# Performance work log

Hardware: AMD Instinct MI355X
Metric: run time of the kernel (lower is better)

The kernel has to match this reference:

```python
import jax, jax.numpy as jnp
import numpy as np

R = 32          # voxel_resolution
GN_GROUPS = 8   # GroupNorm groups used throughout the module


def group_norm(x, scale, bias, groups, eps=1e-5):
    B, C = x.shape[0], x.shape[1]
    spatial = x.shape[2:]
    xg = x.reshape(B, groups, C // groups, -1)
    mu = xg.mean(axis=(2, 3), keepdims=True)
    var = xg.var(axis=(2, 3), keepdims=True)
    xn = ((xg - mu) / jnp.sqrt(var + eps)).reshape((B, C) + spatial)
    sh = (1, C) + (1,) * len(spatial)
    return xn * scale.reshape(sh) + bias.reshape(sh)


def conv3d_same(x, w, b):
    pad = w.shape[-1] // 2
    y = jax.lax.conv_general_dilated(
        x, w, (1, 1, 1), [(pad, pad)] * 3,
        dimension_numbers=('NCDHW', 'OIDHW', 'NCDHW'))
    return y + b.reshape(1, -1, 1, 1, 1)


def _voxelize(coords, features, r):
    # PVCNN Voxelization: center coords, normalize to [0,1], scale to grid,
    # scatter-MEAN point features into a dense [B,C,r,r,r] grid.
    B, C, N = features.shape
    centered = coords - coords.mean(axis=2, keepdims=True)            # [B,3,N]
    norm = jnp.linalg.norm(centered, axis=1, keepdims=True)           # [B,1,N]
    denom = norm.max(axis=2, keepdims=True) * 2.0                     # eps = 0
    nc = centered / denom + 0.5
    nc = jnp.clip(nc * r, 0.0, r - 1.0)                               # float voxel coords
    vi = jnp.round(nc).astype(jnp.int32)                              # [B,3,N]
    flat = (vi[:, 0] * r + vi[:, 1]) * r + vi[:, 2]                   # [B,N]
    seg = (flat + (jnp.arange(B, dtype=jnp.int32) * (r ** 3))[:, None]).reshape(-1)
    feats = features.transpose(0, 2, 1).reshape(B * N, C)
    sums = jax.ops.segment_sum(feats, seg, num_segments=B * r ** 3)
    cnts = jax.ops.segment_sum(jnp.ones((B * N,), feats.dtype), seg,
                               num_segments=B * r ** 3)
    mean = sums / jnp.maximum(cnts, 1.0)[:, None]
    grid = mean.reshape(B, r, r, r, C).transpose(0, 4, 1, 2, 3)       # [B,C,r,r,r]
    return nc, grid


def _trilinear_devoxelize(nc, grid, r):
    # nc [B,3,N] float in [0,r-1]; grid [B,C,r,r,r] -> gather 8 corners + weights
    B, C = grid.shape[0], grid.shape[1]
    lo = jnp.floor(nc)
    frac = nc - lo                                                    # [B,3,N]
    lo_i = lo.astype(jnp.int32)
    hi_i = jnp.minimum(lo_i + 1, r - 1)
    gf = grid.reshape(B, C, r * r * r)
    out = jnp.zeros((B, C, nc.shape[2]), grid.dtype)
    for dx in (0, 1):
        for dy in (0, 1):
            for dz in (0, 1):
                ix = hi_i[:, 0] if dx else lo_i[:, 0]
                iy = hi_i[:, 1] if dy else lo_i[:, 1]
                iz = hi_i[:, 2] if dz else lo_i[:, 2]
                w = ((frac[:, 0] if dx else 1.0 - frac[:, 0]) *
                     (frac[:, 1] if dy else 1.0 - frac[:, 1]) *
                     (frac[:, 2] if dz else 1.0 - frac[:, 2]))        # [B,N]
                idx = (ix * r + iy) * r + iz                          # [B,N]
                g = jnp.take_along_axis(gf, idx[:, None, :], axis=2)  # [B,C,N]
                out = out + g * w[:, None, :]
    return out


def setup_inputs() -> dict:
    key = jax.random.key(0)
    ks = jax.random.split(key, 6)
    B, N, Cin, Cout, K = 4, 65536, 64, 128, 3
    return {
        'coords':   jax.random.normal(ks[0], (B, 3, N), jnp.float32),
        'features': jax.random.normal(ks[1], (B, Cin, N), jnp.float32),
        'conv1_w':  jax.random.normal(ks[2], (Cout, Cin, K, K, K), jnp.float32) * 0.02,
        'conv1_b':  jnp.zeros((Cout,), jnp.float32),
        'gn1_scale': jnp.ones((Cout,), jnp.float32),
        'gn1_bias':  jnp.zeros((Cout,), jnp.float32),
        'conv2_w':  jax.random.normal(ks[3], (Cout, Cout, K, K, K), jnp.float32) * 0.02,
        'conv2_b':  jnp.zeros((Cout,), jnp.float32),
        'gn2_scale': jnp.ones((Cout,), jnp.float32),
        'gn2_bias':  jnp.zeros((Cout,), jnp.float32),
        'point_w':  jax.random.normal(ks[4], (Cout, Cin), jnp.float32) * 0.05,
        'point_b':  jnp.zeros((Cout,), jnp.float32),
        'point_gn_scale': jnp.ones((Cout,), jnp.float32),
        'point_gn_bias':  jnp.zeros((Cout,), jnp.float32),
    }


def reference(coords, features, conv1_w, conv1_b, gn1_scale, gn1_bias,
              conv2_w, conv2_b, gn2_scale, gn2_bias,
              point_w, point_b, point_gn_scale, point_gn_bias):
    nc, grid = _voxelize(coords, features, R)
    # voxel branch: Conv3d -> GN -> SiLU -> (dropout, eval: identity) -> Conv3d -> GN -> SiLU
    h = conv3d_same(grid, conv1_w, conv1_b)
    h = jax.nn.silu(group_norm(h, gn1_scale, gn1_bias, GN_GROUPS))
    h = conv3d_same(h, conv2_w, conv2_b)
    h = jax.nn.silu(group_norm(h, gn2_scale, gn2_bias, GN_GROUPS))
    # point branch: SharedMLP = 1x1 Conv1d -> GN -> SiLU
    p = jnp.einsum('oc,bcn->bon', point_w, features) + point_b[None, :, None]
    p = jax.nn.silu(group_norm(p, point_gn_scale, point_gn_bias, GN_GROUPS))
    vpts = _trilinear_devoxelize(nc, h, R)                            # [B,Cout,N]
    return p + vpts
```

## Files before the change

### kernel.cpp

```cpp
#include <hip/hip_runtime.h>

typedef __attribute__((ext_vector_type(8))) short bf16x8;
typedef __attribute__((ext_vector_type(4))) float f32x4;
typedef __attribute__((ext_vector_type(4))) int i32x4;
typedef __attribute__((ext_vector_type(2))) int i32x2;

#define B_ 4
#define N_ 65536
#define RRR_ 32768
#define PADV_ 39304
#define PPLANE_ 1156

static const size_t OFF_NC     = 0;
static const size_t OFF_VIDX   = 786432;
static const size_t OFF_WT1    = 1048576;
static const size_t OFF_WT2    = 1159168;
static const size_t OFF_C2OUT  = 1380352;
static const size_t OFF_CNT    = 9768960;
static const size_t OFF_GSUM   = 9900032;
static const size_t OFF_GPAD   = 18288640;
static const size_t OFF_ACT1   = 23319552;
static const size_t OFF_GSTATS = 33381376;
static const size_t OFF_BSTATS = 33381568;
static const size_t MEMSET_FLOATS = 33381584 - 9768960;

__device__ __forceinline__ ushort f2bf(float x) {
    union { float f; unsigned u; } c; c.f = x;
    unsigned r = c.u + 0x7fffu + ((c.u >> 16) & 1u);
    return (ushort)(r >> 16);
}
__device__ __forceinline__ float bf2f(ushort h) {
    union { unsigned u; float f; } c; c.u = ((unsigned)h) << 16;
    return c.f;
}

__global__ __launch_bounds__(256) void k_coord_sum(const float* __restrict__ coords,
                                                   float* __restrict__ bstats) {
    int b = blockIdx.y;
    int tid = threadIdx.x;
    const float* cb = coords + (size_t)b * 3 * N_;
    float s0 = 0.f, s1 = 0.f, s2 = 0.f;
    for (int n = blockIdx.x * 256 + tid; n < N_; n += 64 * 256) {
        s0 += cb[n]; s1 += cb[N_ + n]; s2 += cb[2 * N_ + n];
    }
    #pragma unroll
    for (int off = 1; off < 64; off <<= 1) {
        s0 += __shfl_xor(s0, off);
        s1 += __shfl_xor(s1, off);
        s2 += __shfl_xor(s2, off);
    }
    if ((tid & 63) == 0) {
        atomicAdd(&bstats[b * 4 + 0], s0);
        atomicAdd(&bstats[b * 4 + 1], s1);
        atomicAdd(&bstats[b * 4 + 2], s2);
    }
}

__global__ __launch_bounds__(256) void k_coord_max(const float* __restrict__ coords,
                                                   float* __restrict__ bstats) {
    int b = blockIdx.y;
    int tid = threadIdx.x;
    const float invN = 1.0f / (float)N_;
    float m0 = bstats[b * 4 + 0] * invN;
    float m1 = bstats[b * 4 + 1] * invN;
    float m2 = bstats[b * 4 + 2] * invN;
    const float* cb = coords + (size_t)b * 3 * N_;
    float mx = 0.f;
    for (int n = blockIdx.x * 256 + tid; n < N_; n += 64 * 256) {
        float x = cb[n] - m0, y = cb[N_ + n] - m1, z = cb[2 * N_ + n] - m2;
        mx = fmaxf(mx, x * x + y * y + z * z);
    }
    #pragma unroll
    for (int off = 1; off < 64; off <<= 1)
        mx = fmaxf(mx, __shfl_xor(mx, off));
    if ((tid & 63) == 0)
        atomicMax((int*)&bstats[b * 4 + 3], __float_as_int(mx));
}

__global__ __launch_bounds__(256) void k_point_prep(const float* __restrict__ coords,
                                                    const float* __restrict__ bstats,
                                                    float* __restrict__ nc,
                                                    int* __restrict__ vidx,
                                                    float* __restrict__ cnt) {
    int gid = blockIdx.x * 256 + threadIdx.x;
    int b = gid >> 16;
    int n = gid & (N_ - 1);
    const float invN = 1.0f / (float)N_;
    float m[3] = {bstats[b * 4 + 0] * invN, bstats[b * 4 + 1] * invN, bstats[b * 4 + 2] * invN};
    float den = 2.0f * sqrtf(__int_as_float(((const int*)bstats)[b * 4 + 3]));
    const float* cb = coords + (size_t)b * 3 * N_;
    int vi[3];
    #pragma unroll
    for (int d = 0; d < 3; ++d) {
        float cv = cb[(size_t)d * N_ + n];
        float t = (cv - m[d]) / den + 0.5f;
        t *= 32.0f;
        t = fminf(fmaxf(t, 0.0f), 31.0f);
        nc[((size_t)b * 3 + d) * N_ + n] = t;
        vi[d] = (int)rintf(t);
    }
    int flat = (vi[0] * 32 + vi[1]) * 32 + vi[2];
    vidx[(b << 16) + n] = flat;
    atomicAdd(&cnt[(b << 15) + flat], 1.0f);
}

__global__ __launch_bounds__(256) void k_scatter_cl(const float* __restrict__ feats,
                                                    const int* __restrict__ vidx,
                                                    float* __restrict__ gsum) {
    __shared__ float lf[64 * 129];
    __shared__ int sidx[128];
    int tid = threadIdx.x;
    int b = blockIdx.y;
    int n0 = blockIdx.x * 128;
    for (int i = tid; i < 64 * 128; i += 256) {
        int ci = i >> 7, pt = i & 127;
        lf[ci * 129 + pt] = feats[((size_t)(b * 64 + ci)) * N_ + n0 + pt];
    }
    if (tid < 128) sidx[tid] = vidx[(b << 16) + n0 + tid];
    __syncthreads();
    for (int i = tid; i < 64 * 128; i += 256) {
        int ci = i & 63, pt = i >> 6;
        atomicAdd(&gsum[((size_t)(b << 15) + sidx[pt]) * 64 + ci], lf[ci * 129 + pt]);
    }
}

__global__ __launch_bounds__(256) void k_gridmean_cl(const float* __restrict__ gsum,
                                                     const float* __restrict__ cnt,
                                                     ushort* __restrict__ gpad) {
    int idx = blockIdx.x * 256 + threadIdx.x;
    int q = idx & 15;
    int vox = (idx >> 4) & 32767;
    int b = idx >> 19;
    float c = cnt[(b << 15) + vox];
    float inv = 1.0f / fmaxf(c, 1.0f);
    float4 v = *(const float4*)(gsum + (((size_t)(b << 15) + vox) << 6) + q * 4);
    int zz = vox >> 10, yy = (vox >> 5) & 31, xx = vox & 31;
    size_t o = ((size_t)b * PADV_ + (size_t)(zz + 1) * PPLANE_ + (yy + 1) * 34 + (xx + 1)) * 64 + q * 4;
    i32x2 pk;
    ushort* u = (ushort*)&pk;
    u[0] = f2bf(v.x * inv); u[1] = f2bf(v.y * inv);
    u[2] = f2bf(v.z * inv); u[3] = f2bf(v.w * inv);
    *(i32x2*)(gpad + o) = pk;
}

template <int CI>
__global__ __launch_bounds__(256) void k_wtrans(const float* __restrict__ w,
                                                ushort* __restrict__ wt) {
    int idx = blockIdx.x * 256 + threadIdx.x;
    if (idx >= 27 * 128 * CI) return;
    int tap = idx / (128 * CI);
    int rem = idx - tap * 128 * CI;
    int co = rem / CI;
    int ci = rem - co * CI;
    wt[idx] = f2bf(w[((size_t)co * CI + ci) * 27 + tap]);
}

template <int CI, bool PAD_OUT>
__global__ __launch_bounds__(512, 2) void k_conv(const ushort* __restrict__ inp,
                                                 const ushort* __restrict__ wt,
                                                 const float* __restrict__ bias,
                                                 ushort* __restrict__ outp,
                                                 float* __restrict__ gstats,
                                                 int layer) {
    constexpr int NK = 27 * CI / 64;
    __shared__ i32x4 lds_mem[6144];
    char* lds = (char*)lds_mem;

    const int yg = blockIdx.x, z0 = blockIdx.y, b = blockIdx.z;
    const int y0 = yg * 8;
    const int tid = threadIdx.x;
    const int w = tid >> 6, l = tid & 63;
    const int lk = l >> 4, lr = l & 15;
    const int wr = w >> 1, wc = w & 1;

    const ushort* actb = inp + (size_t)b * PADV_ * CI;

    int aglb[4], awld[4];
    #pragma unroll
    for (int i = 0; i < 4; ++i) {
        int idx = tid + i * 512;
        int row = idx >> 3, j = idx & 7;
        int py = row >> 5, px = row & 31;
        aglb[i] = (z0 * PPLANE_ + (y0 + py) * 34 + px) * CI + j * 8;
        awld[i] = row * 128 + ((j ^ (row & 7)) << 4);
    }
    int bglb[2], bwld[2];
    #pragma unroll
    for (int i = 0; i < 2; ++i) {
        int idx = tid + i * 512;
        int co = idx >> 3, j = idx & 7;
        bglb[i] = co * CI + j * 8;
        bwld[i] = co * 128 + ((j ^ (co & 7)) << 4);
    }
    int ard[4][2], brd[4][2];
    #pragma unroll
    for (int i = 0; i < 4; ++i) {
        int pos = wr * 64 + i * 16 + lr;
        #pragma unroll
        for (int kk = 0; kk < 2; ++kk)
            ard[i][kk] = pos * 128 + (((kk * 4 + lk) ^ (pos & 7)) << 4);
    }
    #pragma unroll
    for (int n = 0; n < 4; ++n) {
        int co = wc * 64 + n * 16 + lr;
        #pragma unroll
        for (int kk = 0; kk < 2; ++kk)
            brd[n][kk] = co * 128 + (((kk * 4 + lk) ^ (co & 7)) << 4);
    }

    f32x4 acc[4][4];
    #pragma unroll
    for (int i = 0; i < 4; ++i)
        #pragma unroll
        for (int n = 0; n < 4; ++n)
            acc[i][n] = (f32x4){0.f, 0.f, 0.f, 0.f};

    i32x4 ar[4], br[2];
    #pragma unroll
    for (int i = 0; i < 4; ++i) ar[i] = *(const i32x4*)(actb + aglb[i]);
    #pragma unroll
    for (int i = 0; i < 2; ++i) br[i] = *(const i32x4*)(wt + bglb[i]);
    #pragma unroll
    for (int i = 0; i < 4; ++i) *(i32x4*)(lds + awld[i]) = ar[i];
    #pragma unroll
    for (int i = 0; i < 2; ++i) *(i32x4*)(lds + 65536 + bwld[i]) = br[i];
    __syncthreads();

    #pragma unroll 2
    for (int ks = 0; ks < NK; ++ks) {
        const int cur = ks & 1;
        const bool more = (ks + 1 < NK);
        if (more) {
            int ksn = ks + 1;
            int tap = (CI == 64) ? ksn : (ksn >> 1);
            int choff = (CI == 64) ? 0 : ((ksn & 1) << 6);
            int fz = tap / 9, r9 = tap - fz * 9;
            int fy = r9 / 3, fx = r9 - fy * 3;
            int adelta = (fz * PPLANE_ + fy * 34 + fx) * CI + choff;
            const ushort* wp = wt + tap * (128 * CI) + choff;
            #pragma unroll
            for (int i = 0; i < 4; ++i) ar[i] = *(const i32x4*)(actb + aglb[i] + adelta);
            #pragma unroll
            for (int i = 0; i < 2; ++i) br[i] = *(const i32x4*)(wp + bglb[i]);
        }
        const char* Ac = lds + cur * 32768;
        const char* Bc = lds + 65536 + cur * 16384;
        #pragma unroll
        for (int kk = 0; kk < 2; ++kk) {
            bf16x8 af[4], bfr[4];
            #pragma unroll
            for (int i = 0; i < 4; ++i) af[i] = *(const bf16x8*)(Ac + ard[i][kk]);
            #pragma unroll
            for (int n = 0; n < 4; ++n) bfr[n] = *(const bf16x8*)(Bc + brd[n][kk]);
            #pragma unroll
            for (int i = 0; i < 4; ++i)
                #pragma unroll
                for (int n = 0; n < 4; ++n)
                    acc[i][n] = __builtin_amdgcn_mfma_f32_16x16x32_bf16(af[i], bfr[n], acc[i][n], 0, 0, 0);
        }
        if (more) {
            char* An = lds + (cur ^ 1) * 32768;
            char* Bn = lds + 65536 + (cur ^ 1) * 16384;
            #pragma unroll
            for (int i = 0; i < 4; ++i) *(i32x4*)(An + awld[i]) = ar[i];
            #pragma unroll
            for (int i = 0; i < 2; ++i) *(i32x4*)(Bn + bwld[i]) = br[i];
            __syncthreads();
        }
    }

    __syncthreads();
    ushort* outs = (ushort*)lds;
    float bb[4];
    #pragma unroll
    for (int n = 0; n < 4; ++n) bb[n] = bias[wc * 64 + n * 16 + lr];
    float sg[4] = {0.f, 0.f, 0.f, 0.f}, sq[4] = {0.f, 0.f, 0.f, 0.f};
    #pragma unroll
    for (int i = 0; i < 4; ++i) {
        int posb = wr * 64 + i * 16 + lk * 4;
        #pragma unroll
        for (int n = 0; n < 4; ++n) {
            int co = wc * 64 + n * 16 + lr;
            #pragma unroll
            for (int r = 0; r < 4; ++r) {
                float v = acc[i][n][r] + bb[n];
                sg[n] += v; sq[n] += v * v;
                outs[(posb + r) * 128 + co] = f2bf(v);
            }
        }
    }
    #pragma unroll
    for (int off = 1; off < 64; off <<= 1) {
        #pragma unroll
        for (int n = 0; n < 4; ++n) {
            sg[n] += __shfl_xor(sg[n], off);
            sq[n] += __shfl_xor(sq[n], off);
        }
    }
    if (l == 0) {
        int gbase = layer * 32 + b * 8 + wc * 4;
        #pragma unroll
        for (int n = 0; n < 4; ++n) {
            atomicAdd(&gstats[(gbase + n) * 2 + 0], sg[n]);
            atomicAdd(&gstats[(gbase + n) * 2 + 1], sq[n]);
        }
    }
    __syncthreads();
    for (int idx = tid; idx < 4096; idx += 512) {
        int pos = idx >> 4, c8 = idx & 15;
        int yy = y0 + (pos >> 5), xx = pos & 31;
        size_t g;
        if (PAD_OUT)
            g = ((size_t)b * PADV_ + (size_t)(z0 + 1) * PPLANE_ + (yy + 1) * 34 + (xx + 1)) * 128 + c8 * 8;
        else
            g = ((size_t)b * RRR_ + z0 * 1024 + yy * 32 + xx) * 128 + c8 * 8;
        *(i32x4*)(outp + g) = *((i32x4*)lds + idx);
    }
}

template <bool PAD>
__global__ __launch_bounds__(256) void k_gn_apply(ushort* __restrict__ x,
                                                  const float* __restrict__ gstats,
                                                  const float* __restrict__ sc,
                                                  const float* __restrict__ bi,
                                                  int layer, float invc) {
    int idx = blockIdx.x * 256 + threadIdx.x;
    int c8 = idx & 15;
    int vox = (idx >> 4) & 32767;
    int b = idx >> 19;
    size_t base;
    if (PAD) {
        int zz = vox >> 10, yy = (vox >> 5) & 31, xx = vox & 31;
        base = ((size_t)b * PADV_ + (size_t)(zz + 1) * PPLANE_ + (yy + 1) * 34 + (xx + 1)) * 128 + c8 * 8;
    } else {
        base = ((size_t)b * RRR_ + vox) * 128 + c8 * 8;
    }
    int g = c8 >> 1;
    float sum = gstats[(layer * 32 + b * 8 + g) * 2 + 0];
    float ssq = gstats[(layer * 32 + b * 8 + g) * 2 + 1];
    float mean = sum * invc;
    float var = ssq * invc - mean * mean;
    float rstd = rsqrtf(var + 1e-5f);
    i32x4 raw = *(i32x4*)(x + base);
    ushort* u = (ushort*)&raw;
    #pragma unroll
    for (int j = 0; j < 8; ++j) {
        int co = c8 * 8 + j;
        float v = bf2f(u[j]);
        v = (v - mean) * rstd * sc[co] + bi[co];
        v = v / (1.f + __expf(-v));
        u[j] = f2bf(v);
    }
    *(i32x4*)(x + base) = raw;
}

__global__ __launch_bounds__(256) void k_point_mlp(const float* __restrict__ feats,
                                                   const float* __restrict__ w,
                                                   const float* __restrict__ pb,
                                                   float* __restrict__ out,
                                                   float* __restrict__ gstats) {
    __shared__ float wl[64 * 132];
    __shared__ float sred[4][16];
    int tid = threadIdx.x;
    for (int i = tid; i < 128 * 64; i += 256) {
        int o = i >> 6, c = i & 63;
        wl[c * 132 + o] = w[i];
    }
    __syncthreads();
    int gid = blockIdx.x * 256 + tid;
    int b = gid >> 16, n = gid & (N_ - 1);
    const float* fb = feats + (size_t)b * 64 * N_ + n;
    float acc[128];
    #pragma unroll
    for (int o = 0; o < 128; ++o) acc[o] = 0.f;
    for (int c = 0; c < 64; ++c) {
        float f = fb[(size_t)c * N_];
        const float4* wr4 = (const float4*)&wl[c * 132];
        #pragma unroll
        for (int o4 = 0; o4 < 32; ++o4) {
            float4 wv = wr4[o4];
            acc[4 * o4 + 0] = fmaf(f, wv.x, acc[4 * o4 + 0]);
            acc[4 * o4 + 1] = fmaf(f, wv.y, acc[4 * o4 + 1]);
            acc[4 * o4 + 2] = fmaf(f, wv.z, acc[4 * o4 + 2]);
            acc[4 * o4 + 3] = fmaf(f, wv.w, acc[4 * o4 + 3]);
        }
    }
    float* ob = out + (size_t)b * 128 * N_ + n;
    float sg[8] = {0.f}, sq[8] = {0.f};
    #pragma unroll
    for (int o = 0; o < 128; ++o) {
        float v = acc[o] + pb[o];
        ob[(size_t)o * N_] = v;
        sg[o >> 4] += v;
        sq[o >> 4] += v * v;
    }
    #pragma unroll
    for (int off = 1; off < 64; off <<= 1) {
        #pragma unroll
        for (int g = 0; g < 8; ++g) {
            sg[g] += __shfl_xor(sg[g], off);
            sq[g] += __shfl_xor(sq[g], off);
        }
    }
    int wv = tid >> 6, l = tid & 63;
    if (l == 0) {
        #pragma unroll
        for (int g = 0; g < 8; ++g) { sred[wv][g] = sg[g]; sred[wv][8 + g] = sq[g]; }
    }
    __syncthreads();
    if (tid < 16) {
        float v = sred[0][tid] + sred[1][tid] + sred[2][tid] + sred[3][tid];
        int g = tid & 7, part = tid >> 3;
        atomicAdd(&gstats[(64 + b * 8 + g) * 2 + part], v);
    }
}

__global__ __launch_bounds__(256) void k_devox_final(const float* __restrict__ nc,
                                                     const ushort* __restrict__ ht,
                                                     const float* __restrict__ gstats,
                                                     const float* __restrict__ scale,
                                                     const float* __restrict__ bias,
                                                     float* __restrict__ out) {
    __shared__ float vp[64][129];
    __shared__ int sidx[64][8];
    __shared__ float swt[64][8];
    int tid = threadIdx.x;
    int blk = blockIdx.x;
    int b = blk >> 10;
    int n0 = (blk & 1023) * 64;
    if (tid < 64) {
        int n = n0 + tid;
        float f0 = nc[(size_t)b * 3 * N_ + n];
        float f1 = nc[((size_t)b * 3 + 1) * N_ + n];
        float f2 = nc[((size_t)b * 3 + 2) * N_ + n];
        float l0 = floorf(f0), l1 = floorf(f1), l2 = floorf(f2);
        float r0 = f0 - l0, r1 = f1 - l1, r2 = f2 - l2;
        int i0 = (int)l0, i1 = (int)l1, i2 = (int)l2;
        int h0 = min(i0 + 1, 31), h1 = min(i1 + 1, 31), h2 = min(i2 + 1, 31);
        #pragma unroll
        for (int k = 0; k < 8; ++k) {
            int dx = (k >> 2) & 1, dy = (k >> 1) & 1, dz = k & 1;
            int ix = dx ? h0 : i0, iy = dy ? h1 : i1, iz = dz ? h2 : i2;
            float w = (dx ? r0 : 1.f - r0) * (dy ? r1 : 1.f - r1) * (dz ? r2 : 1.f - r2);
            sidx[tid][k] = (ix * 32 + iy) * 32 + iz;
            swt[tid][k] = w;
        }
    }
    __syncthreads();
    const ushort* hb = ht + (size_t)b * RRR_ * 128;
    for (int t = tid; t < 64 * 16; t += 256) {
        int c8 = t & 15, pt = t >> 4;
        float a[8] = {0.f, 0.f, 0.f, 0.f, 0.f, 0.f, 0.f, 0.f};
        #pragma unroll
        for (int k = 0; k < 8; ++k) {
            i32x4 raw = *(const i32x4*)(hb + (size_t)sidx[pt][k] * 128 + c8 * 8);
            ushort* u = (ushort*)&raw;
            float wk = swt[pt][k];
            #pragma unroll
            for (int j = 0; j < 8; ++j)
                a[j] = fmaf(wk, bf2f(u[j]), a[j]);
        }
        #pragma unroll
        for (int j = 0; j < 8; ++j)
            vp[pt][c8 * 8 + j] = a[j];
    }
    __syncthreads();
    const float invc = 1.0f / (16.0f * (float)N_);
    for (int t = tid; t < 64 * 128; t += 256) {
        int nl = t & 63;
        int c = t >> 6;
        int g = c >> 4;
        float sum = gstats[(64 + b * 8 + g) * 2 + 0];
        float ssq = gstats[(64 + b * 8 + g) * 2 + 1];
        float mean = sum * invc;
        float var = ssq * invc - mean * mean;
        float rstd = rsqrtf(var + 1e-5f);
        size_t o = ((size_t)(b * 128 + c)) * N_ + n0 + nl;
        float v = (out[o] - mean) * rstd * scale[c] + bias[c];
        v = v / (1.f + __expf(-v));
        out[o] = v + vp[nl][c];
    }
}

extern "C" void kernel_launch(void* const* d_in, const int* in_sizes, int n_in,
                              void* d_out, int out_size, void* d_ws, size_t ws_size,
                              hipStream_t stream) {
    const float* coords   = (const float*)d_in[0];
    const float* features = (const float*)d_in[1];
    const float* conv1_w  = (const float*)d_in[2];
    const float* conv1_b  = (const float*)d_in[3];
    const float* gn1_s    = (const float*)d_in[4];
    const float* gn1_b    = (const float*)d_in[5];
    const float* conv2_w  = (const float*)d_in[6];
    const float* conv2_b  = (const float*)d_in[7];
    const float* gn2_s    = (const float*)d_in[8];
    const float* gn2_b    = (const float*)d_in[9];
    const float* point_w  = (const float*)d_in[10];
    const float* point_b  = (const float*)d_in[11];
    const float* pgn_s    = (const float*)d_in[12];
    const float* pgn_b    = (const float*)d_in[13];
    float* out = (float*)d_out;
    float* ws = (float*)d_ws;

    float*  nc     = ws + OFF_NC;
    int*    vidx   = (int*)(ws + OFF_VIDX);
    ushort* wt1    = (ushort*)(ws + OFF_WT1);
    ushort* wt2    = (ushort*)(ws + OFF_WT2);
    ushort* c2out  = (ushort*)(ws + OFF_C2OUT);
    float*  cnt    = ws + OFF_CNT;
    float*  gsum   = ws + OFF_GSUM;
    ushort* gpad   = (ushort*)(ws + OFF_GPAD);
    ushort* act1   = (ushort*)(ws + OFF_ACT1);
    float*  gstats = ws + OFF_GSTATS;
    float*  bstats = ws + OFF_BSTATS;

    const float invc = 1.0f / (float)(RRR_ * 16);

    hipMemsetAsync(cnt, 0, MEMSET_FLOATS * sizeof(float), stream);

    k_coord_sum<<<dim3(64, B_), 256, 0, stream>>>(coords, bstats);
    k_coord_max<<<dim3(64, B_), 256, 0, stream>>>(coords, bstats);
    k_point_prep<<<B_ * N_ / 256, 256, 0, stream>>>(coords, bstats, nc, vidx, cnt);
    k_scatter_cl<<<dim3(N_ / 128, B_), 256, 0, stream>>>(features, vidx, gsum);
    k_gridmean_cl<<<B_ * RRR_ * 16 / 256, 256, 0, stream>>>(gsum, cnt, gpad);

    k_wtrans<64><<<(27 * 128 * 64 + 255) / 256, 256, 0, stream>>>(conv1_w, wt1);
    k_wtrans<128><<<(27 * 128 * 128 + 255) / 256, 256, 0, stream>>>(conv2_w, wt2);

    k_conv<64, true><<<dim3(4, 32, B_), 512, 0, stream>>>(gpad, wt1, conv1_b, act1, gstats, 0);
    k_gn_apply<true><<<B_ * RRR_ * 16 / 256, 256, 0, stream>>>(act1, gstats, gn1_s, gn1_b, 0, invc);

    k_conv<128, false><<<dim3(4, 32, B_), 512, 0, stream>>>(act1, wt2, conv2_b, c2out, gstats, 1);
    k_gn_apply<false><<<B_ * RRR_ * 16 / 256, 256, 0, stream>>>(c2out, gstats, gn2_s, gn2_b, 1, invc);

    k_point_mlp<<<B_ * N_ / 256, 256, 0, stream>>>(features, point_w, point_b, out, gstats);
    k_devox_final<<<B_ * N_ / 64, 256, 0, stream>>>(nc, c2out, gstats, pgn_s, pgn_b, out);
}
```

Before: 1.011 ms.

## Stage conv tiles via direct global-to-LDS loads with pre-swizzled weights

The implicit-GEMM 3D conv now loads activation and weight tiles directly into LDS with global_load_lds instead of staging them through registers. Weights are pre-arranged in the XOR-swizzled order so each thread copies a contiguous 16-byte chunk. The block tile drops from 256 to 128 positions with 256 threads, halving LDS use and doubling the grid. This removes register staging and LDS store instructions, but relies on vmcnt waits plus a barrier every k-step and gives less reuse of each weight tile per block.

```diff
diff --git a/kernel.cpp b/kernel.cpp
--- a/kernel.cpp
+++ b/kernel.cpp
@@ -32,6 +32,13 @@
 __device__ __forceinline__ float bf2f(ushort h) {
     union { unsigned u; float f; } c; c.u = ((unsigned)h) << 16;
     return c.f;
+}
+
+__device__ __forceinline__ void gl16(const void* g, void* l) {
+    __builtin_amdgcn_global_load_lds(
+        (const __attribute__((address_space(1))) unsigned int*)(g),
+        (__attribute__((address_space(3))) unsigned int*)(l),
+        16, 0, 0);
 }
 
 __global__ __launch_bounds__(256) void k_coord_sum(const float* __restrict__ coords,
@@ -148,50 +155,48 @@
                                                 ushort* __restrict__ wt) {
     int idx = blockIdx.x * 256 + threadIdx.x;
     if (idx >= 27 * 128 * CI) return;
-    int tap = idx / (128 * CI);
-    int rem = idx - tap * 128 * CI;
-    int co = rem / CI;
-    int ci = rem - co * CI;
+    int e = idx & 7;
+    int jm = (idx >> 3) & 7;
+    int co = (idx >> 6) & 127;
+    int ks = idx >> 13;
+    int q = jm ^ (co & 7);
+    int tap = (CI == 64) ? ks : (ks >> 1);
+    int ci = ((CI == 64) ? 0 : ((ks & 1) * 64)) + q * 8 + e;
     wt[idx] = f2bf(w[((size_t)co * CI + ci) * 27 + tap]);
 }
 
 template <int CI, bool PAD_OUT>
-__global__ __launch_bounds__(512, 2) void k_conv(const ushort* __restrict__ inp,
+__global__ __launch_bounds__(256, 2) void k_conv(const ushort* __restrict__ inp,
                                                  const ushort* __restrict__ wt,
                                                  const float* __restrict__ bias,
                                                  ushort* __restrict__ outp,
                                                  float* __restrict__ gstats,
                                                  int layer) {
     constexpr int NK = 27 * CI / 64;
-    __shared__ i32x4 lds_mem[6144];
-    char* lds = (char*)lds_mem;
+    __shared__ char lds[65536];
 
     const int yg = blockIdx.x, z0 = blockIdx.y, b = blockIdx.z;
-    const int y0 = yg * 8;
+    const int y0 = yg * 4;
     const int tid = threadIdx.x;
     const int w = tid >> 6, l = tid & 63;
     const int lk = l >> 4, lr = l & 15;
     const int wr = w >> 1, wc = w & 1;
 
-    const ushort* actb = inp + (size_t)b * PADV_ * CI;
-
-    int aglb[4], awld[4];
+    const char* actb = (const char*)(inp + (size_t)b * PADV_ * CI);
+    const char* wtb = (const char*)wt;
+
+    const char* agp[4];
     #pragma unroll
     for (int i = 0; i < 4; ++i) {
-        int idx = tid + i * 512;
-        int row = idx >> 3, j = idx & 7;
+        int s = tid + i * 256;
+        int row = s >> 3, j = s & 7;
+        int jj = j ^ (row & 7);
         int py = row >> 5, px = row & 31;
-        aglb[i] = (z0 * PPLANE_ + (y0 + py) * 34 + px) * CI + j * 8;
-        awld[i] = row * 128 + ((j ^ (row & 7)) << 4);
-    }
-    int bglb[2], bwld[2];
-    #pragma unroll
-    for (int i = 0; i < 2; ++i) {
-        int idx = tid + i * 512;
-        int co = idx >> 3, j = idx & 7;
-        bglb[i] = co * CI + j * 8;
-        bwld[i] = co * 128 + ((j ^ (co & 7)) << 4);
-    }
+        agp[i] = actb + ((size_t)(z0 * PPLANE_ + (y0 + py) * 34 + px) * CI) * 2 + jj * 16;
+    }
+    char* ldsAw = lds + w * 1024;
+    char* ldsBw = lds + 32768 + w * 1024;
+
     int ard[4][2], brd[4][2];
     #pragma unroll
     for (int i = 0; i < 4; ++i) {
@@ -215,36 +220,31 @@
         for (int n = 0; n < 4; ++n)
             acc[i][n] = (f32x4){0.f, 0.f, 0.f, 0.f};
 
-    i32x4 ar[4], br[2];
-    #pragma unroll
-    for (int i = 0; i < 4; ++i) ar[i] = *(const i32x4*)(actb + aglb[i]);
-    #pragma unroll
-    for (int i = 0; i < 2; ++i) br[i] = *(const i32x4*)(wt + bglb[i]);
-    #pragma unroll
-    for (int i = 0; i < 4; ++i) *(i32x4*)(lds + awld[i]) = ar[i];
-    #pragma unroll
-    for (int i = 0; i < 2; ++i) *(i32x4*)(lds + 65536 + bwld[i]) = br[i];
+    auto stage = [&](int ks, int cur) {
+        int tap = (CI == 64) ? ks : (ks >> 1);
+        int choff2 = (CI == 64) ? 0 : ((ks & 1) << 7);
+        int fz = tap / 9, r9 = tap - fz * 9;
+        int fy = r9 / 3, fx = r9 - fy * 3;
+        int ad = (fz * PPLANE_ + fy * 34 + fx) * CI * 2 + choff2;
+        #pragma unroll
+        for (int i = 0; i < 4; ++i)
+            gl16(agp[i] + ad, ldsAw + cur * 16384 + i * 4096);
+        const char* wsrc = wtb + (size_t)ks * 16384 + tid * 16;
+        #pragma unroll
+        for (int i = 0; i < 4; ++i)
+            gl16(wsrc + i * 4096, ldsBw + cur * 16384 + i * 4096);
+    };
+
+    stage(0, 0);
+    asm volatile("s_waitcnt vmcnt(0)" ::: "memory");
     __syncthreads();
 
     #pragma unroll 2
     for (int ks = 0; ks < NK; ++ks) {
         const int cur = ks & 1;
-        const bool more = (ks + 1 < NK);
-        if (more) {
-            int ksn = ks + 1;
-            int tap = (CI == 64) ? ksn : (ksn >> 1);
-            int choff = (CI == 64) ? 0 : ((ksn & 1) << 6);
-            int fz = tap / 9, r9 = tap - fz * 9;
-            int fy = r9 / 3, fx = r9 - fy * 3;
-            int adelta = (fz * PPLANE_ + fy * 34 + fx) * CI + choff;
-            const ushort* wp = wt + tap * (128 * CI) + choff;
-            #pragma unroll
-            for (int i = 0; i < 4; ++i) ar[i] = *(const i32x4*)(actb + aglb[i] + adelta);
-            #pragma unroll
-            for (int i = 0; i < 2; ++i) br[i] = *(const i32x4*)(wp + bglb[i]);
-        }
-        const char* Ac = lds + cur * 32768;
-        const char* Bc = lds + 65536 + cur * 16384;
+        if (ks + 1 < NK) stage(ks + 1, cur ^ 1);
+        const char* Ac = lds + cur * 16384;
+        const char* Bc = lds + 32768 + cur * 16384;
         #pragma unroll
         for (int kk = 0; kk < 2; ++kk) {
             bf16x8 af[4], bfr[4];
@@ -258,18 +258,10 @@
                 for (int n = 0; n < 4; ++n)
                     acc[i][n] = __builtin_amdgcn_mfma_f32_16x16x32_bf16(af[i], bfr[n], acc[i][n], 0, 0, 0);
         }
-        if (more) {
-            char* An = lds + (cur ^ 1) * 32768;
-            char* Bn = lds + 65536 + (cur ^ 1) * 16384;
-            #pragma unroll
-            for (int i = 0; i < 4; ++i) *(i32x4*)(An + awld[i]) = ar[i];
-            #pragma unroll
-            for (int i = 0; i < 2; ++i) *(i32x4*)(Bn + bwld[i]) = br[i];
-            __syncthreads();
-        }
-    }
-
-    __syncthreads();
+        asm volatile("s_waitcnt vmcnt(0)" ::: "memory");
+        __syncthreads();
+    }
+
     ushort* outs = (ushort*)lds;
     float bb[4];
     #pragma unroll
@@ -306,7 +298,7 @@
         }
     }
     __syncthreads();
-    for (int idx = tid; idx < 4096; idx += 512) {
+    for (int idx = tid; idx < 2048; idx += 256) {
         int pos = idx >> 4, c8 = idx & 15;
         int yy = y0 + (pos >> 5), xx = pos & 31;
         size_t g;
@@ -527,10 +519,10 @@
     k_wtrans<64><<<(27 * 128 * 64 + 255) / 256, 256, 0, stream>>>(conv1_w, wt1);
     k_wtrans<128><<<(27 * 128 * 128 + 255) / 256, 256, 0, stream>>>(conv2_w, wt2);
 
-    k_conv<64, true><<<dim3(4, 32, B_), 512, 0, stream>>>(gpad, wt1, conv1_b, act1, gstats, 0);
+    k_conv<64, true><<<dim3(8, 32, B_), 256, 0, stream>>>(gpad, wt1, conv1_b, act1, gstats, 0);
     k_gn_apply<true><<<B_ * RRR_ * 16 / 256, 256, 0, stream>>>(act1, gstats, gn1_s, gn1_b, 0, invc);
 
-    k_conv<128, false><<<dim3(4, 32, B_), 512, 0, stream>>>(act1, wt2, conv2_b, c2out, gstats, 1);
+    k_conv<128, false><<<dim3(8, 32, B_), 256, 0, stream>>>(act1, wt2, conv2_b, c2out, gstats, 1);
     k_gn_apply<false><<<B_ * RRR_ * 16 / 256, 256, 0, stream>>>(c2out, gstats, gn2_s, gn2_b, 1, invc);
 
     k_point_mlp<<<B_ * N_ / 256, 256, 0, stream>>>(features, point_w, point_b, out, gstats);
```

After: 1.124 ms. 11.1% more time.
